# Optimization experiments

Measured on AMD Instinct MI355X. Metric: run time of the kernel, lower is better.

## Reference

```python
import jax, jax.numpy as jnp
import numpy as np

B, S, H, C = 256, 512, 1024, 10

def setup_inputs() -> dict:
    key = jax.random.key(0)
    ks = jax.random.split(key, 10)
    sx = 1.0 / np.sqrt((H + 1) / 2.0)   # xavier-normal-ish scale for [H,1]
    sh = 1.0 / np.sqrt(H)
    inp = {
        "x": jax.random.normal(ks[0], (B, S), dtype=jnp.float32),
        "w_gx": jax.random.normal(ks[1], (H, 1), dtype=jnp.float32) * sx,
        "w_ix": jax.random.normal(ks[2], (H, 1), dtype=jnp.float32) * sx,
        "w_fx": jax.random.normal(ks[3], (H, 1), dtype=jnp.float32) * sx,
        "w_ox": jax.random.normal(ks[4], (H, 1), dtype=jnp.float32) * sx,
        "w_gh": jax.random.normal(ks[5], (H, H), dtype=jnp.float32) * sh,
        "w_ih": jax.random.normal(ks[6], (H, H), dtype=jnp.float32) * sh,
        "w_fh": jax.random.normal(ks[7], (H, H), dtype=jnp.float32) * sh,
        "w_oh": jax.random.normal(ks[8], (H, H), dtype=jnp.float32) * sh,
        "w_ph": jax.random.normal(ks[9], (C, H), dtype=jnp.float32) * sh,
        "b_g": jnp.zeros((H,), jnp.float32),
        "b_i": jnp.zeros((H,), jnp.float32),
        "b_f": jnp.zeros((H,), jnp.float32),
        "b_o": jnp.zeros((H,), jnp.float32),
        "b_p": jnp.zeros((C,), jnp.float32),
    }
    return inp

def reference(x, w_gx, w_ix, w_fx, w_ox, w_gh, w_ih, w_fh, w_oh, w_ph,
              b_g, b_i, b_f, b_o, b_p):
    Bn = x.shape[0]
    Hn = w_gh.shape[0]
    h0 = jnp.zeros((Bn, Hn), x.dtype)
    c0 = jnp.zeros((Bn, Hn), x.dtype)

    def step(carry, xt):
        h, c = carry
        xt = xt[:, None]  # [B, 1], input_dim == 1
        g = jnp.tanh(xt @ w_gx.T + h @ w_gh.T + b_g)
        i = jax.nn.sigmoid(xt @ w_ix.T + h @ w_ih.T + b_i)
        f = jax.nn.sigmoid(xt @ w_fx.T + h @ w_fh.T + b_f)
        o = jax.nn.sigmoid(xt @ w_ox.T + h @ w_oh.T + b_o)
        c_new = g * i + c * f
        h_new = jnp.tanh(c_new) * o
        return (h_new, c_new), None

    (hT, _), _ = jax.lax.scan(step, (h0, c0), x.T)  # scan over time: [S, B]
    return hT @ w_ph.T + b_p  # [B, num_classes]
```

## Files before the change

kernel.cpp:

```cpp
#include <hip/hip_runtime.h>
#include <hip/hip_bf16.h>

#define B_ 256
#define S_ 512
#define H_ 1024
#define C_ 10

typedef unsigned long long u64;
typedef __attribute__((ext_vector_type(8))) short s8v;
typedef __attribute__((ext_vector_type(4))) float f4v;


__global__ void prep_w(const float* __restrict__ wg, const float* __restrict__ wi,
                       const float* __restrict__ wf, const float* __restrict__ wo,
                       __hip_bfloat16* __restrict__ Wp) {
    int idx = blockIdx.x * 256 + threadIdx.x;
    int g   = idx >> 17;
    int rem = idx & 131071;
    int o   = rem >> 7;
    int kg  = rem & 127;
    const float* src = (g == 0 ? wg : g == 1 ? wi : g == 2 ? wf : wo) + o * H_ + kg * 8;
    int kc   = kg >> 2;
    int quad = kg & 3;
    int lane = quad * 16 + (o & 15);
    int ot   = o >> 4;
    int blk  = (g * 64 + ot) * 32 + kc;
    __hip_bfloat16* dst = Wp + blk * 512 + lane * 8;
#pragma unroll
    for (int j = 0; j < 8; ++j) dst[j] = __float2bfloat16(src[j]);
}

__global__ void prep_x(const float* __restrict__ x, float* __restrict__ xT) {
    int i = blockIdx.x * 256 + threadIdx.x;
    int t = i >> 8, b = i & 255;
    xT[i] = x[b * S_ + t];
}

__device__ __forceinline__ float sigmoid_f(float x) { return 1.0f / (1.0f + __expf(-x)); }
__device__ __forceinline__ float tanh_f(float x)    { return 2.0f / (1.0f + __expf(-2.0f * x)) - 1.0f; }

__device__ __forceinline__ float bf2f(unsigned short u) {
    union { unsigned i; float f; } x; x.i = ((unsigned)u) << 16; return x.f;
}
__device__ __forceinline__ unsigned short f2bf(float f) {
    union { __hip_bfloat16 h; unsigned short s; } x; x.h = __float2bfloat16(f); return x.s;
}

#define LOADH(kc, g, off)                                                        \
    asm volatile("global_load_dwordx4 %0, %1, off offset:" #off " sc0 sc1"       \
                 : "=v"(hfrag[kc]) : "v"(hb[g]));

#define WAITV(n)                                                                 \
    asm volatile("s_waitcnt vmcnt(" #n ")" ::: "memory");                        \
    __builtin_amdgcn_sched_barrier(0);

#define MM(kc) {                                                                 \
    s8v hv = hfrag[kc];                                                          \
    acc0 = __builtin_amdgcn_mfma_f32_16x16x32_bf16(Wlds[0 * 2048 + (kc) * 64 + l], hv, acc0, 0, 0, 0); \
    acc1 = __builtin_amdgcn_mfma_f32_16x16x32_bf16(Wlds[1 * 2048 + (kc) * 64 + l], hv, acc1, 0, 0, 0); \
    acc2 = __builtin_amdgcn_mfma_f32_16x16x32_bf16(Wlds[2 * 2048 + (kc) * 64 + l], hv, acc2, 0, 0, 0); \
    acc3 = __builtin_amdgcn_mfma_f32_16x16x32_bf16(Wlds[3 * 2048 + (kc) * 64 + l], hv, acc3, 0, 0, 0); }

__global__ __launch_bounds__(256, 1) void lstm_main(
    const float* __restrict__ xT,
    const float* __restrict__ wgx, const float* __restrict__ wix,
    const float* __restrict__ wfx, const float* __restrict__ wox,
    const float* __restrict__ bg,  const float* __restrict__ bi,
    const float* __restrict__ bf,  const float* __restrict__ bo,
    const __hip_bfloat16* __restrict__ Wp,
    __hip_bfloat16* __restrict__ h0, __hip_bfloat16* __restrict__ h1,
    const float* __restrict__ wph, const float* __restrict__ bp,
    float* __restrict__ out,
    unsigned* __restrict__ flags)
{
    __shared__ s8v Wlds[4 * 32 * 64];
    __shared__ unsigned done_cnt;
    __shared__ unsigned tok;

    const int tid  = threadIdx.x;
    const int wgid = blockIdx.x;
    const int m    = wgid >> 6;
    const int n    = wgid & 63;
    const int w    = tid >> 6;
    const int l    = tid & 63;
    const int quad = l >> 4;
    const int l16  = l & 15;
    const int b    = m * 64 + w * 16 + l16;
    const int out0 = n * 16 + quad * 4;

    if (tid == 0) { done_cnt = 0u; tok = 0u; }

    {
        const s8v* Wv = (const s8v*)Wp;
#pragma unroll
        for (int j = 0; j < 32; ++j) {
            int idx = j * 256 + tid;
            int g   = idx >> 11;
            int rem = idx & 2047;
            Wlds[g * 2048 + rem] = Wv[((g * 64 + n) * 32) * 64 + rem];
        }
    }

    float wxg[4], wxi[4], wxf[4], wxo[4], bbg[4], bbi[4], bbf[4], bbo[4];
    *(float4*)wxg = *(const float4*)(wgx + out0);
    *(float4*)wxi = *(const float4*)(wix + out0);
    *(float4*)wxf = *(const float4*)(wfx + out0);
    *(float4*)wxo = *(const float4*)(wox + out0);
    *(float4*)bbg = *(const float4*)(bg + out0);
    *(float4*)bbi = *(const float4*)(bi + out0);
    *(float4*)bbf = *(const float4*)(bf + out0);
    *(float4*)bbo = *(const float4*)(bo + out0);

    float cs[4] = {0.f, 0.f, 0.f, 0.f};

    const unsigned* flp = flags + (u64)(m * 64 + l) * 32;
    unsigned* myflag    = flags + (u64)(m * 64 + n) * 32;

    const u64 tbOff = (u64)((m * 4 + w) * 32768) + (u64)l * 16;
    const int eidx_s = ((m * 4 + w) * 32 + (out0 >> 5)) * 64 + ((out0 >> 3) & 3) * 16 + l16;
    const u64 stOff  = (u64)eidx_s * 16 + (u64)(out0 & 7) * 2;
    u64 xaddr = (u64)(const void*)xT + (u64)b * 4;
    const u64 h0a = (u64)(const void*)h0;
    const u64 h1a = (u64)(const void*)h1;

    __syncthreads();

    float xa_cur, xa_nxt;
    asm volatile("global_load_dword %0, %1, off" : "=v"(xa_cur) : "v"(xaddr));

    for (int t = 0; t < S_; ++t) {
        const unsigned tu = (unsigned)t;
        const u64 hinB  = (t & 1) ? h1a : h0a;
        const u64 houtB = (t & 1) ? h0a : h1a;

        if (w == 0) {
            for (;;) {
                unsigned v = __hip_atomic_load(flp, __ATOMIC_RELAXED,
                                               __HIP_MEMORY_SCOPE_AGENT);
                if ((__ballot(v < tu) & 0xFFFFFFFFull) == 0ull) break;
                __builtin_amdgcn_s_sleep(1);
            }
            if (l == 0)
                __hip_atomic_store(&tok, 2u * tu + 1u, __ATOMIC_RELAXED,
                                   __HIP_MEMORY_SCOPE_WORKGROUP);
        } else {
            while (__hip_atomic_load(&tok, __ATOMIC_RELAXED,
                                     __HIP_MEMORY_SCOPE_WORKGROUP) < 2u * tu + 1u) { }
        }
        __builtin_amdgcn_sched_barrier(0);

        u64 hb[8];
        u64 base = hinB + tbOff;
#pragma unroll
        for (int g = 0; g < 8; ++g) hb[g] = base + (u64)g * 4096;

        s8v hfrag[32];
        LOADH( 0, 0, 0) LOADH( 1, 0, 1024) LOADH( 2, 0, 2048) LOADH( 3, 0, 3072)
        LOADH( 4, 1, 0) LOADH( 5, 1, 1024) LOADH( 6, 1, 2048) LOADH( 7, 1, 3072)
        LOADH( 8, 2, 0) LOADH( 9, 2, 1024) LOADH(10, 2, 2048) LOADH(11, 2, 3072)
        LOADH(12, 3, 0) LOADH(13, 3, 1024) LOADH(14, 3, 2048) LOADH(15, 3, 3072)

        if (w == 0) {
            for (;;) {
                unsigned v = __hip_atomic_load(flp, __ATOMIC_RELAXED,
                                               __HIP_MEMORY_SCOPE_AGENT);
                if (__ballot(v < tu) == 0ull) break;
                __builtin_amdgcn_s_sleep(1);
            }
            if (l == 0)
                __hip_atomic_store(&tok, 2u * tu + 2u, __ATOMIC_RELAXED,
                                   __HIP_MEMORY_SCOPE_WORKGROUP);
        } else {
            while (__hip_atomic_load(&tok, __ATOMIC_RELAXED,
                                     __HIP_MEMORY_SCOPE_WORKGROUP) < 2u * tu + 2u) { }
        }
        __builtin_amdgcn_sched_barrier(0);

        LOADH(16, 4, 0) LOADH(17, 4, 1024) LOADH(18, 4, 2048) LOADH(19, 4, 3072)
        LOADH(20, 5, 0) LOADH(21, 5, 1024) LOADH(22, 5, 2048) LOADH(23, 5, 3072)
        LOADH(24, 6, 0) LOADH(25, 6, 1024) LOADH(26, 6, 2048) LOADH(27, 6, 3072)
        LOADH(28, 7, 0) LOADH(29, 7, 1024) LOADH(30, 7, 2048) LOADH(31, 7, 3072)

        f4v acc0 = {0.f, 0.f, 0.f, 0.f}, acc1 = acc0, acc2 = acc0, acc3 = acc0;
        WAITV(24)
        MM(0)  MM(1)  MM(2)  MM(3)  MM(4)  MM(5)  MM(6)  MM(7)
        WAITV(16)
        MM(8)  MM(9)  MM(10) MM(11) MM(12) MM(13) MM(14) MM(15)
        WAITV(8)
        MM(16) MM(17) MM(18) MM(19) MM(20) MM(21) MM(22) MM(23)
        WAITV(0)
        MM(24) MM(25) MM(26) MM(27) MM(28) MM(29) MM(30) MM(31)

        float xa = xa_cur;
        unsigned short hs[4];
#pragma unroll
        for (int r = 0; r < 4; ++r) {
            float pg = acc0[r] + xa * wxg[r] + bbg[r];
            float pi = acc1[r] + xa * wxi[r] + bbi[r];
            float pf = acc2[r] + xa * wxf[r] + bbf[r];
            float po = acc3[r] + xa * wxo[r] + bbo[r];
            float gv = tanh_f(pg);
            float iv = sigmoid_f(pi);
            float fv = sigmoid_f(pf);
            float ov = sigmoid_f(po);
            float cn = gv * iv + cs[r] * fv;
            cs[r] = cn;
            hs[r] = f2bf(tanh_f(cn) * ov);
        }
        union { unsigned short s[4]; u64 q; } hp_;
        hp_.s[0] = hs[0]; hp_.s[1] = hs[1]; hp_.s[2] = hs[2]; hp_.s[3] = hs[3];
        __hip_atomic_store((u64*)(houtB + stOff), hp_.q,
                           __ATOMIC_RELAXED, __HIP_MEMORY_SCOPE_AGENT);

        xaddr += (u64)B_ * 4;
        asm volatile("global_load_dword %0, %1, off" : "=v"(xa_nxt) : "v"(xaddr));

        asm volatile("s_waitcnt vmcnt(0)" ::: "memory");
        if (l == 0) {
            unsigned old = __hip_atomic_fetch_add(&done_cnt, 1u, __ATOMIC_RELAXED,
                                                  __HIP_MEMORY_SCOPE_WORKGROUP);
            if (old == 4u * tu + 3u)
                __hip_atomic_store(myflag, tu + 1u, __ATOMIC_RELAXED,
                                   __HIP_MEMORY_SCOPE_AGENT);
        }
        xa_cur = xa_nxt;
    }

    if (w == 0) {
        for (;;) {
            unsigned v = __hip_atomic_load(flp, __ATOMIC_RELAXED,
                                           __HIP_MEMORY_SCOPE_AGENT);
            if (__ballot(v < (unsigned)S_) == 0ull) break;
            __builtin_amdgcn_s_sleep(1);
        }
        if (l == 0)
            __hip_atomic_store(&tok, 2u * (unsigned)S_ + 1u, __ATOMIC_RELAXED,
                               __HIP_MEMORY_SCOPE_WORKGROUP);
    }
    while (__hip_atomic_load(&tok, __ATOMIC_RELAXED,
                             __HIP_MEMORY_SCOPE_WORKGROUP) < 2u * (unsigned)S_ + 1u) { }
    __builtin_amdgcn_sched_barrier(0);

    const __hip_bfloat16* hf = h0;
    int wig = n * 4 + w;
    for (int p = wig; p < 64 * C_; p += 256) {
        int row = m * 64 + p / C_;
        int cc  = p % C_;
        int tb  = row >> 4, bl = row & 15;
        const float* wr = wph + cc * H_;
        float acc = 0.f;
#pragma unroll
        for (int j = 0; j < 4; ++j) {
            int k   = j * 256 + l * 4;
            int kc  = k >> 5;
            int qd  = (k >> 3) & 3;
            const u64* hp = (const u64*)((const char*)hf
                              + ((size_t)((tb * 32 + kc) * 64 + qd * 16 + bl)) * 16
                              + (size_t)(k & 7) * 2);
            u64 hv4 = __hip_atomic_load(hp, __ATOMIC_RELAXED, __HIP_MEMORY_SCOPE_AGENT);
            union { u64 q; unsigned short s[4]; } u_; u_.q = hv4;
            float4 wv = *(const float4*)(wr + k);
            acc += bf2f(u_.s[0]) * wv.x + bf2f(u_.s[1]) * wv.y
                 + bf2f(u_.s[2]) * wv.z + bf2f(u_.s[3]) * wv.w;
        }
#pragma unroll
        for (int off = 32; off > 0; off >>= 1) acc += __shfl_down(acc, off, 64);
        if (l == 0) out[row * C_ + cc] = acc + bp[cc];
    }
}

extern "C" void kernel_launch(void* const* d_in, const int* in_sizes, int n_in,
                              void* d_out, int out_size, void* d_ws, size_t ws_size,
                              hipStream_t stream) {
    const float* x   = (const float*)d_in[0];
    const float* wgx = (const float*)d_in[1];
    const float* wix = (const float*)d_in[2];
    const float* wfx = (const float*)d_in[3];
    const float* wox = (const float*)d_in[4];
    const float* wgh = (const float*)d_in[5];
    const float* wih = (const float*)d_in[6];
    const float* wfh = (const float*)d_in[7];
    const float* woh = (const float*)d_in[8];
    const float* wph = (const float*)d_in[9];
    const float* bg  = (const float*)d_in[10];
    const float* bi  = (const float*)d_in[11];
    const float* bf  = (const float*)d_in[12];
    const float* bo  = (const float*)d_in[13];
    const float* bp  = (const float*)d_in[14];
    float* out = (float*)d_out;

    char* ws = (char*)d_ws;
    unsigned*       flags = (unsigned*)ws;
    float*          xT    = (float*)(ws + 32768);
    __hip_bfloat16* h0    = (__hip_bfloat16*)(ws + 32768 + 524288);
    __hip_bfloat16* h1    = (__hip_bfloat16*)(ws + 32768 + 2 * 524288);
    __hip_bfloat16* Wp    = (__hip_bfloat16*)(ws + 32768 + 3 * 524288);

    hipMemsetAsync(flags, 0, 32768, stream);
    hipMemsetAsync(h0, 0, 524288, stream);
    prep_x<<<512, 256, 0, stream>>>(x, xT);
    prep_w<<<2048, 256, 0, stream>>>(wgh, wih, wfh, woh, Wp);
    lstm_main<<<256, 256, 0, stream>>>(xT, wgx, wix, wfx, wox, bg, bi, bf, bo,
                                       Wp, h0, h1, wph, bp, out, flags);
}
```

Baseline: 3.052 ms.

## Use per-wave flags with vector polling and overlap partial MFMA with second barrier wait

Each wave now publishes its own completion flag, replacing the shared-memory done counter. Pollers read all four wave flags of a peer with one dwordx4 load and no sleep. The second-half barrier wait moves to wave 3, so the other waves start MFMAs on the first-half h fragments before the wait completes. The intent is to cut the inter-workgroup handoff latency in each recurrent step, at the cost of more global polling traffic and a subtler memory-ordering scheme.

```diff
diff --git a/kernel.cpp b/kernel.cpp
--- a/kernel.cpp
+++ b/kernel.cpp
@@ -9,6 +9,7 @@
 typedef unsigned long long u64;
 typedef __attribute__((ext_vector_type(8))) short s8v;
 typedef __attribute__((ext_vector_type(4))) float f4v;
+typedef __attribute__((ext_vector_type(4))) unsigned u4v;
 
 
 __global__ void prep_w(const float* __restrict__ wg, const float* __restrict__ wi,
@@ -61,6 +62,14 @@
     acc2 = __builtin_amdgcn_mfma_f32_16x16x32_bf16(Wlds[2 * 2048 + (kc) * 64 + l], hv, acc2, 0, 0, 0); \
     acc3 = __builtin_amdgcn_mfma_f32_16x16x32_bf16(Wlds[3 * 2048 + (kc) * 64 + l], hv, acc3, 0, 0, 0); }
 
+#define POLL4(mnvar)                                                             \
+    u4v f4_;                                                                     \
+    asm volatile("global_load_dwordx4 %0, %1, off sc0 sc1\n\t"                   \
+                 "s_waitcnt vmcnt(0)" : "=v"(f4_) : "v"(flpa));                  \
+    unsigned a_ = f4_.x < f4_.y ? f4_.x : f4_.y;                                 \
+    unsigned b_ = f4_.z < f4_.w ? f4_.z : f4_.w;                                 \
+    unsigned mnvar = a_ < b_ ? a_ : b_;
+
 __global__ __launch_bounds__(256, 1) void lstm_main(
     const float* __restrict__ xT,
     const float* __restrict__ wgx, const float* __restrict__ wix,
@@ -74,7 +83,6 @@
     unsigned* __restrict__ flags)
 {
     __shared__ s8v Wlds[4 * 32 * 64];
-    __shared__ unsigned done_cnt;
     __shared__ unsigned tok;
 
     const int tid  = threadIdx.x;
@@ -88,7 +96,7 @@
     const int b    = m * 64 + w * 16 + l16;
     const int out0 = n * 16 + quad * 4;
 
-    if (tid == 0) { done_cnt = 0u; tok = 0u; }
+    if (tid == 0) tok = 0u;
 
     {
         const s8v* Wv = (const s8v*)Wp;
@@ -113,8 +121,8 @@
 
     float cs[4] = {0.f, 0.f, 0.f, 0.f};
 
-    const unsigned* flp = flags + (u64)(m * 64 + l) * 32;
-    unsigned* myflag    = flags + (u64)(m * 64 + n) * 32;
+    const u64 flpa   = (u64)(const void*)(flags + (u64)(m * 64 + l) * 32);
+    unsigned* myflag = flags + (u64)(m * 64 + n) * 32 + w;
 
     const u64 tbOff = (u64)((m * 4 + w) * 32768) + (u64)l * 16;
     const int eidx_s = ((m * 4 + w) * 32 + (out0 >> 5)) * 64 + ((out0 >> 3) & 3) * 16 + l16;
@@ -125,8 +133,8 @@
 
     __syncthreads();
 
-    float xa_cur, xa_nxt;
-    asm volatile("global_load_dword %0, %1, off" : "=v"(xa_cur) : "v"(xaddr));
+    float xa_nxt;
+    asm volatile("global_load_dword %0, %1, off" : "=v"(xa_nxt) : "v"(xaddr));
 
     for (int t = 0; t < S_; ++t) {
         const unsigned tu = (unsigned)t;
@@ -135,10 +143,8 @@
 
         if (w == 0) {
             for (;;) {
-                unsigned v = __hip_atomic_load(flp, __ATOMIC_RELAXED,
-                                               __HIP_MEMORY_SCOPE_AGENT);
-                if ((__ballot(v < tu) & 0xFFFFFFFFull) == 0ull) break;
-                __builtin_amdgcn_s_sleep(1);
+                POLL4(mn)
+                if ((__ballot(mn < tu) & 0xFFFFFFFFull) == 0ull) break;
             }
             if (l == 0)
                 __hip_atomic_store(&tok, 2u * tu + 1u, __ATOMIC_RELAXED,
@@ -160,38 +166,46 @@
         LOADH( 8, 2, 0) LOADH( 9, 2, 1024) LOADH(10, 2, 2048) LOADH(11, 2, 3072)
         LOADH(12, 3, 0) LOADH(13, 3, 1024) LOADH(14, 3, 2048) LOADH(15, 3, 3072)
 
-        if (w == 0) {
+        f4v acc0 = {0.f, 0.f, 0.f, 0.f}, acc1 = acc0, acc2 = acc0, acc3 = acc0;
+
+        if (w == 3) {
             for (;;) {
-                unsigned v = __hip_atomic_load(flp, __ATOMIC_RELAXED,
-                                               __HIP_MEMORY_SCOPE_AGENT);
-                if (__ballot(v < tu) == 0ull) break;
-                __builtin_amdgcn_s_sleep(1);
+                POLL4(mn)
+                if (__ballot(mn < tu) == 0ull) break;
             }
             if (l == 0)
                 __hip_atomic_store(&tok, 2u * tu + 2u, __ATOMIC_RELAXED,
                                    __HIP_MEMORY_SCOPE_WORKGROUP);
+            __builtin_amdgcn_sched_barrier(0);
+            LOADH(16, 4, 0) LOADH(17, 4, 1024) LOADH(18, 4, 2048) LOADH(19, 4, 3072)
+            LOADH(20, 5, 0) LOADH(21, 5, 1024) LOADH(22, 5, 2048) LOADH(23, 5, 3072)
+            LOADH(24, 6, 0) LOADH(25, 6, 1024) LOADH(26, 6, 2048) LOADH(27, 6, 3072)
+            LOADH(28, 7, 0) LOADH(29, 7, 1024) LOADH(30, 7, 2048) LOADH(31, 7, 3072)
+            MM(0)  MM(1)  MM(2)  MM(3)  MM(4)  MM(5)  MM(6)  MM(7)
+            MM(8)  MM(9)  MM(10) MM(11) MM(12) MM(13) MM(14) MM(15)
+            WAITV(8)
+            MM(16) MM(17) MM(18) MM(19) MM(20) MM(21) MM(22) MM(23)
+            WAITV(0)
+            MM(24) MM(25) MM(26) MM(27) MM(28) MM(29) MM(30) MM(31)
         } else {
+            WAITV(8)
+            MM(0)  MM(1)  MM(2)  MM(3)  MM(4)  MM(5)  MM(6)  MM(7)
             while (__hip_atomic_load(&tok, __ATOMIC_RELAXED,
                                      __HIP_MEMORY_SCOPE_WORKGROUP) < 2u * tu + 2u) { }
-        }
-        __builtin_amdgcn_sched_barrier(0);
-
-        LOADH(16, 4, 0) LOADH(17, 4, 1024) LOADH(18, 4, 2048) LOADH(19, 4, 3072)
-        LOADH(20, 5, 0) LOADH(21, 5, 1024) LOADH(22, 5, 2048) LOADH(23, 5, 3072)
-        LOADH(24, 6, 0) LOADH(25, 6, 1024) LOADH(26, 6, 2048) LOADH(27, 6, 3072)
-        LOADH(28, 7, 0) LOADH(29, 7, 1024) LOADH(30, 7, 2048) LOADH(31, 7, 3072)
-
-        f4v acc0 = {0.f, 0.f, 0.f, 0.f}, acc1 = acc0, acc2 = acc0, acc3 = acc0;
-        WAITV(24)
-        MM(0)  MM(1)  MM(2)  MM(3)  MM(4)  MM(5)  MM(6)  MM(7)
-        WAITV(16)
-        MM(8)  MM(9)  MM(10) MM(11) MM(12) MM(13) MM(14) MM(15)
-        WAITV(8)
-        MM(16) MM(17) MM(18) MM(19) MM(20) MM(21) MM(22) MM(23)
-        WAITV(0)
-        MM(24) MM(25) MM(26) MM(27) MM(28) MM(29) MM(30) MM(31)
-
-        float xa = xa_cur;
+            __builtin_amdgcn_sched_barrier(0);
+            LOADH(16, 4, 0) LOADH(17, 4, 1024) LOADH(18, 4, 2048) LOADH(19, 4, 3072)
+            LOADH(20, 5, 0) LOADH(21, 5, 1024) LOADH(22, 5, 2048) LOADH(23, 5, 3072)
+            LOADH(24, 6, 0) LOADH(25, 6, 1024) LOADH(26, 6, 2048) LOADH(27, 6, 3072)
+            LOADH(28, 7, 0) LOADH(29, 7, 1024) LOADH(30, 7, 2048) LOADH(31, 7, 3072)
+            WAITV(16)
+            MM(8)  MM(9)  MM(10) MM(11) MM(12) MM(13) MM(14) MM(15)
+            WAITV(8)
+            MM(16) MM(17) MM(18) MM(19) MM(20) MM(21) MM(22) MM(23)
+            WAITV(0)
+            MM(24) MM(25) MM(26) MM(27) MM(28) MM(29) MM(30) MM(31)
+        }
+
+        float xa = xa_nxt;
         unsigned short hs[4];
 #pragma unroll
         for (int r = 0; r < 4; ++r) {
@@ -212,26 +226,16 @@
         __hip_atomic_store((u64*)(houtB + stOff), hp_.q,
                            __ATOMIC_RELAXED, __HIP_MEMORY_SCOPE_AGENT);
 
+        WAITV(0)
+        __hip_atomic_store(myflag, tu + 1u, __ATOMIC_RELAXED, __HIP_MEMORY_SCOPE_AGENT);
         xaddr += (u64)B_ * 4;
         asm volatile("global_load_dword %0, %1, off" : "=v"(xa_nxt) : "v"(xaddr));
-
-        asm volatile("s_waitcnt vmcnt(0)" ::: "memory");
-        if (l == 0) {
-            unsigned old = __hip_atomic_fetch_add(&done_cnt, 1u, __ATOMIC_RELAXED,
-                                                  __HIP_MEMORY_SCOPE_WORKGROUP);
-            if (old == 4u * tu + 3u)
-                __hip_atomic_store(myflag, tu + 1u, __ATOMIC_RELAXED,
-                                   __HIP_MEMORY_SCOPE_AGENT);
-        }
-        xa_cur = xa_nxt;
     }
 
     if (w == 0) {
         for (;;) {
-            unsigned v = __hip_atomic_load(flp, __ATOMIC_RELAXED,
-                                           __HIP_MEMORY_SCOPE_AGENT);
-            if (__ballot(v < (unsigned)S_) == 0ull) break;
-            __builtin_amdgcn_s_sleep(1);
+            POLL4(mn)
+            if (__ballot(mn < (unsigned)S_) == 0ull) break;
         }
         if (l == 0)
             __hip_atomic_store(&tok, 2u * (unsigned)S_ + 1u, __ATOMIC_RELAXED,
```

Result: slower. 3.500 ms (+14.7%).
